# Optimization experiments

Hardware: AMD Instinct MI355X
Metric: run time of the kernel (lower is better)

The kernel has to match this reference:

```python
import jax, jax.numpy as jnp
import numpy as np

H = 512; VT = 10000; VN = 1000; ET = 256; EN = 256
A = 50; B = 8; L = 128; SOS = 0


def setup_inputs():
    key = jax.random.key(0)
    ks = jax.random.split(key, 12)
    g = lambda k, s: jax.random.normal(k, s, jnp.float32) * 0.02
    inp = {}
    inp["n_tensor"] = jax.random.randint(ks[0], (B, L), 0, VN)
    inp["t_tensor"] = jax.random.randint(ks[1], (B, L), 0, VT)
    inp["p_tensor"] = jax.random.randint(ks[2], (B, L), 0, L)
    # embedding tables; padding rows (padding_idx) zeroed as nn.Embedding init does
    inp["embN"] = g(ks[3], (VN, EN)).at[VN - 1].set(0.0)
    inp["embT"] = g(ks[4], (VT + A + 3, ET)).at[VT - 1].set(0.0)
    inp["W_hid"] = g(ks[5], (H, H)); inp["b_hid"] = jnp.zeros((H,), jnp.float32)
    inp["W_mem"] = g(ks[6], (H, H)); inp["b_mem"] = jnp.zeros((H,), jnp.float32)
    inp["v_w"] = g(ks[7], (H,)); inp["v_b"] = jnp.zeros((), jnp.float32)
    inp["W_ih"] = g(ks[8], (4 * H, EN + ET)); inp["W_hh"] = g(ks[9], (4 * H, H))
    inp["b_ih"] = jnp.zeros((4 * H,), jnp.float32); inp["b_hh"] = jnp.zeros((4 * H,), jnp.float32)
    inp["W_g"] = g(ks[10], (3 * H, VT + 3)); inp["b_g"] = jnp.zeros((VT + 3,), jnp.float32)
    inp["W_s"] = g(ks[11], (2 * H,)); inp["b_s"] = jnp.zeros((), jnp.float32)
    return inp


def _forward(embN, embT, W_hid, b_hid, W_mem, b_mem, v_w, v_b,
             W_ih, W_hh, b_ih, b_hh, W_g, b_g, W_s, b_s,
             n_tensor, t_tensor, p_tensor):
    full_mask = (n_tensor == VN - 1)                      # [B, L] eof mask
    sos = jnp.full((B, 1), SOS, n_tensor.dtype)
    n_in = jnp.concatenate([sos, n_tensor[:, :-1]], 1)    # teacher-forced inputs
    t_in = jnp.concatenate([sos, t_tensor[:, :-1]], 1)
    par = jnp.concatenate([jnp.zeros((B, 1), p_tensor.dtype), p_tensor[:, :-1]], 1)
    hs0 = jnp.zeros((B, L, H), jnp.float32)               # growing memory buffer
    h0 = jnp.zeros((B, H), jnp.float32)
    c0 = jnp.zeros((B, H), jnp.float32)
    barange = jnp.arange(B)
    arangeA = jnp.arange(A)

    def step(carry, xs):
        hs, h, c = carry
        t, n_t, t_t, p_t, tgt = xs
        # embedding gathers + single-layer LSTM cell (torch gate order i,f,g,o)
        x = jnp.concatenate([embN[n_t], embT[t_t]], 1)    # [B, EN+ET]
        gates = x @ W_ih.T + h @ W_hh.T + (b_ih + b_hh)
        i, f, gg, o = jnp.split(gates, 4, axis=1)
        c = jax.nn.sigmoid(f) * c + jax.nn.sigmoid(i) * jnp.tanh(gg)
        h = jax.nn.sigmoid(o) * jnp.tanh(c)
        # sliding-window memory hs[:, max(t-A,0):t], fixed-size slice + validity mask
        s = jnp.maximum(t - A, 0)
        mem = jax.lax.dynamic_slice(hs, (0, s, 0), (B, A, H))   # [B, A, H]
        fm = jax.lax.dynamic_slice(full_mask, (0, s), (B, A))   # [B, A]
        valid = (s + arangeA) < t                               # [A] positions already written
        mask = fm | ~valid[None, :]
        # additive attention: v^T tanh(W_hid h + W_mem mem)
        sc = jnp.tanh((h @ W_hid.T + b_hid)[:, None, :] + mem @ W_mem.T + b_mem)
        sc = sc @ v_w + v_b                                     # [B, A]
        sc = jnp.where(mask, -1e20, sc)
        attn = jax.nn.softmax(sc, axis=1)
        context = jnp.einsum('ba,bah->bh', attn, mem)
        h_parent = hs[barange, p_t]                             # per-batch gather on memory
        wt = jax.nn.log_softmax(jnp.concatenate([context, h, h_parent], 1) @ W_g + b_g, axis=1)
        log_attn = jax.nn.log_softmax(sc, axis=1)
        st = jax.nn.log_sigmoid(jnp.concatenate([context, h], 1) @ W_s + b_s)[:, None]  # [B,1]
        out = jnp.concatenate(
            [st + wt, jnp.log(jnp.clip(-jnp.expm1(st), 1e-18, 1e18)) + log_attn], 1)    # [B, VT+3+A]
        hs = hs.at[:, t].set(h)                                 # scatter new hidden into buffer
        loss_t = -jnp.take_along_axis(out, tgt[:, None], axis=1)[:, 0]  # NLLLoss(reduction='none')
        pred = jnp.argmax(out, axis=1)
        return (hs, h, c), (loss_t, pred)

    ts = jnp.arange(L)
    _, (losses, preds) = jax.lax.scan(
        step, (hs0, h0, c0), (ts, n_in.T, t_in.T, par.T, t_tensor.T))
    return losses.sum(), preds.T


def reference(n_tensor, t_tensor, p_tensor, embN, embT, W_hid, b_hid, W_mem, b_mem,
              v_w, v_b, W_ih, W_hh, b_ih, b_hh, W_g, b_g, W_s, b_s):
    return _forward(embN, embT, W_hid, b_hid, W_mem, b_mem, v_w, v_b,
                    W_ih, W_hh, b_ih, b_hh, W_g, b_g, W_s, b_s,
                    n_tensor, t_tensor, p_tensor)
```

## Files before the change

kernel.cpp:

```cpp
#include <hip/hip_runtime.h>
#include <hip/hip_bf16.h>
#include <math.h>

#define H_ 512
#define VN_ 1000
#define NG_ 10003
#define NGP_ 10240
#define NCHUNK 40
#define A_ 50
#define B_ 8
#define L_ 128
#define R_ 1024

typedef __hip_bfloat16 bf16;
typedef __attribute__((ext_vector_type(8))) short bf16x8;
typedef __attribute__((ext_vector_type(4))) float f32x4;

typedef union { unsigned long long u[2]; bf16x8 v; } frag_u;

__device__ __forceinline__ float fsig(float x) { return 1.0f / (1.0f + __expf(-x)); }
__device__ __forceinline__ float ftanh(float x) { return 1.0f - 2.0f / (1.0f + __expf(2.0f * x)); }

__device__ __forceinline__ short b16(float v) {
    __hip_bfloat16 h = __float2bfloat16(v);
    return *(short*)&h;
}

__device__ __forceinline__ unsigned long long ald(const unsigned long long* p) {
    return __hip_atomic_load(p, __ATOMIC_RELAXED, __HIP_MEMORY_SCOPE_AGENT);
}
__device__ __forceinline__ void ast32(unsigned int* p, unsigned int v) {
    __hip_atomic_store(p, v, __ATOMIC_RELAXED, __HIP_MEMORY_SCOPE_AGENT);
}

__global__ void k_init(int* flags, float* bkq,
                       const float* __restrict__ bmem, const float* __restrict__ bhid,
                       float* out)
{
    int i = blockIdx.x * 256 + threadIdx.x;
    if (i < 32)
        __hip_atomic_store(&flags[i], 0, __ATOMIC_RELAXED, __HIP_MEMORY_SCOPE_AGENT);
    if (i < 512) bkq[i] = bmem[i];
    else if (i < 1024) bkq[i] = bhid[i - 512];
    if (i == 0) out[0] = 0.f;
}

__global__ void k_w2b(const float* __restrict__ src, bf16* __restrict__ dst, int n)
{
    for (int i = blockIdx.x * blockDim.x + threadIdx.x; i < n; i += gridDim.x * blockDim.x)
        dst[i] = __float2bfloat16(src[i]);
}

__global__ void k_embed(const int* __restrict__ nt, const int* __restrict__ tt,
                        const float* __restrict__ embN, const float* __restrict__ embT,
                        bf16* __restrict__ X)
{
    int i = blockIdx.x * blockDim.x + threadIdx.x;
    int r = i >> 9, k = i & 511;
    int t = r >> 3, b = r & 7;
    float v;
    if (k < 256) {
        int id = (t == 0) ? 0 : nt[b * L_ + t - 1];
        v = embN[id * 256 + k];
    } else {
        int id = (t == 0) ? 0 : tt[b * L_ + t - 1];
        v = embT[id * 256 + (k - 256)];
    }
    X[i] = __float2bfloat16(v);
}

#define LSTM_BLOCKS 16
#define XTRA 240

#define DECLW(i) bf16x8 Wa##i, Wb##i;
#define LOADW(i) { \
    float4 a0 = *(const float4*)(wr0 + (i)*32); \
    float4 a1 = *(const float4*)(wr0 + (i)*32 + 4); \
    float4 c0 = *(const float4*)(wr1 + (i)*32); \
    float4 c1 = *(const float4*)(wr1 + (i)*32 + 4); \
    Wa##i[0]=b16(a0.x); Wa##i[1]=b16(a0.y); Wa##i[2]=b16(a0.z); Wa##i[3]=b16(a0.w); \
    Wa##i[4]=b16(a1.x); Wa##i[5]=b16(a1.y); Wa##i[6]=b16(a1.z); Wa##i[7]=b16(a1.w); \
    Wb##i[0]=b16(c0.x); Wb##i[1]=b16(c0.y); Wb##i[2]=b16(c0.z); Wb##i[3]=b16(c0.w); \
    Wb##i[4]=b16(c1.x); Wb##i[5]=b16(c1.y); Wb##i[6]=b16(c1.z); Wb##i[7]=b16(c1.w); }
#define LDF(i) frag_u fu##i; fu##i.u[0] = ald(src + (i)*128); fu##i.u[1] = ald(src + (i)*128 + 1);
#define MM(i) \
    acc0 = __builtin_amdgcn_mfma_f32_16x16x32_bf16(Wa##i, fu##i.v, acc0, 0, 0, 0); \
    acc1 = __builtin_amdgcn_mfma_f32_16x16x32_bf16(Wb##i, fu##i.v, acc1, 0, 0, 0);

__launch_bounds__(256, 1)
__global__ void k_lstm(const float* __restrict__ Whh, const float* __restrict__ xg,
                       bf16* __restrict__ hsb,
                       unsigned long long* __restrict__ bfr, int* __restrict__ flags,
                       const float* __restrict__ Wg, bf16* __restrict__ WT,
                       const float* __restrict__ Wmem, const float* __restrict__ Whid,
                       bf16* __restrict__ wkq)
{
    __shared__ float gl[4][32][9];
    __shared__ short S[64][65];
    const int tid  = threadIdx.x;
    const int x    = blockIdx.x;

    if (x >= LSTM_BLOCKS) {
        for (int i = (x - LSTM_BLOCKS) * 256 + tid; i < 2 * 512 * 512; i += XTRA * 256) {
            float v = (i < 512 * 512) ? Wmem[i] : Whid[i - 512 * 512];
            wkq[i] = __float2bfloat16(v);
        }
        const int c = tid & 63;
        const int r0 = (tid >> 6) * 16;
        const int n_l = tid >> 2;
        const int kq = (tid & 3) * 16;
        for (int tile = x - LSTM_BLOCKS; tile < 160 * 24; tile += XTRA) {
            int n0 = (tile % 160) * 64, k0 = (tile / 160) * 64;
            __syncthreads();
            #pragma unroll
            for (int i = 0; i < 16; ++i) {
                int k = r0 + i;
                int n = n0 + c;
                float v = (n < NG_) ? Wg[(size_t)(k0 + k) * NG_ + n] : 0.f;
                S[c][k] = b16(v);
            }
            __syncthreads();
            bf16* dst = WT + (size_t)(n0 + n_l) * 1536 + k0 + kq;
            #pragma unroll
            for (int j = 0; j < 2; ++j) {
                bf16x8 v;
                #pragma unroll
                for (int e = 0; e < 8; ++e) v[e] = S[n_l][kq + j * 8 + e];
                *(bf16x8*)(dst + j * 8) = v;
            }
        }
        return;
    }

    const int lane = tid & 63;
    const int w    = tid >> 6;
    const int m_l  = lane & 15;
    const int kg   = lane >> 4;
    const int n    = lane & 15;
    unsigned int* bfr32 = (unsigned int*)bfr;

    const float* wr0 = Whh + (size_t)(w * 512 + x * 32 + m_l) * 512 + kg * 8;
    const float* wr1 = wr0 + (size_t)16 * 512;
    DECLW(0)  DECLW(1)  DECLW(2)  DECLW(3)  DECLW(4)  DECLW(5)  DECLW(6)  DECLW(7)
    DECLW(8)  DECLW(9)  DECLW(10) DECLW(11) DECLW(12) DECLW(13) DECLW(14) DECLW(15)
    LOADW(0)  LOADW(1)  LOADW(2)  LOADW(3)  LOADW(4)  LOADW(5)  LOADW(6)  LOADW(7)
    LOADW(8)  LOADW(9)  LOADW(10) LOADW(11) LOADW(12) LOADW(13) LOADW(14) LOADW(15)
    asm volatile("" : "+v"(Wa0), "+v"(Wb0), "+v"(Wa1), "+v"(Wb1), "+v"(Wa2), "+v"(Wb2),
                      "+v"(Wa3), "+v"(Wb3), "+v"(Wa4), "+v"(Wb4), "+v"(Wa5), "+v"(Wb5),
                      "+v"(Wa6), "+v"(Wb6), "+v"(Wa7), "+v"(Wb7));
    asm volatile("" : "+v"(Wa8), "+v"(Wb8), "+v"(Wa9), "+v"(Wb9), "+v"(Wa10), "+v"(Wb10),
                      "+v"(Wa11), "+v"(Wb11), "+v"(Wa12), "+v"(Wb12), "+v"(Wa13), "+v"(Wb13),
                      "+v"(Wa14), "+v"(Wb14), "+v"(Wa15), "+v"(Wb15));

    const int u_l = tid >> 3;
    const int b   = tid & 7;
    float creg = 0.f;
    int fearly = 0;

    for (int t = 0; t < L_; ++t) {
        const float* xr = xg + ((size_t)t * B_ + b) * 2048 + x * 32 + u_l;
        float xi = xr[0], xf = xr[512], xgg = xr[1024], xo = xr[1536];

        f32x4 acc0 = {0.f, 0.f, 0.f, 0.f};
        f32x4 acc1 = {0.f, 0.f, 0.f, 0.f};
        if (t > 0) {
            if (!__all(fearly >= t)) {
                for (;;) {
                    int v = (lane < LSTM_BLOCKS)
                        ? __hip_atomic_load(&flags[lane], __ATOMIC_RELAXED, __HIP_MEMORY_SCOPE_AGENT)
                        : t;
                    if (__all(v >= t)) break;
                    __builtin_amdgcn_s_sleep(1);
                }
            }
            const unsigned long long* src =
                bfr + (size_t)((t + 1) & 1) * 2048 + lane * 2;
            LDF(0)  LDF(1)  LDF(2)  LDF(3)  LDF(4)  LDF(5)  LDF(6)  LDF(7)
            LDF(8)  LDF(9)  LDF(10) LDF(11) LDF(12) LDF(13) LDF(14) LDF(15)
            __builtin_amdgcn_sched_barrier(0);
            MM(0)  MM(1)  MM(2)  MM(3)  MM(4)  MM(5)  MM(6)  MM(7)
            MM(8)  MM(9)  MM(10) MM(11) MM(12) MM(13) MM(14) MM(15)
        }
        if (n < 8) {
            #pragma unroll
            for (int i = 0; i < 4; ++i) {
                gl[w][kg * 4 + i][n]      = acc0[i];
                gl[w][16 + kg * 4 + i][n] = acc1[i];
            }
        }
        __syncthreads();
        float gi = gl[0][u_l][b] + xi;
        float gf = gl[1][u_l][b] + xf;
        float gg = gl[2][u_l][b] + xgg;
        float go = gl[3][u_l][b] + xo;
        float iv = fsig(gi), fv = fsig(gf), gv = ftanh(gg), ov = fsig(go);
        creg = fv * creg + iv * gv;
        float h = ov * ftanh(creg);
        float h2 = __shfl_xor(h, 8);
        unsigned pay = 0;
        if ((u_l & 1) == 0) {
            pay = (unsigned)(unsigned short)b16(h)
                | ((unsigned)(unsigned short)b16(h2) << 16);
            int q = u_l >> 3, p = (u_l & 7) >> 1;
            ast32(bfr32 + (size_t)(t & 1) * 4096 + x * 256 + (b + 16 * q) * 4 + p, pay);
        }
        fearly = (lane < LSTM_BLOCKS && lane != x)
            ? __hip_atomic_load(&flags[lane], __ATOMIC_RELAXED, __HIP_MEMORY_SCOPE_AGENT)
            : 0x7FFFFFFF;
        asm volatile("s_waitcnt vmcnt(0)" ::: "memory");
        __syncthreads();
        if (tid == 0)
            __hip_atomic_store(&flags[x], t + 1, __ATOMIC_RELAXED, __HIP_MEMORY_SCOPE_AGENT);
        if ((u_l & 1) == 0)
            *(unsigned int*)(hsb + (size_t)(t * B_ + b) * 512 + x * 32 + u_l) = pay;
    }
}

__launch_bounds__(256)
__global__ void k_attn(const bf16* __restrict__ hsb, const float* __restrict__ kmq,
                       const float* __restrict__ vw,
                       const float* __restrict__ vb, const int* __restrict__ nt,
                       const int* __restrict__ pt, const float* __restrict__ Wsv,
                       const float* __restrict__ bs, bf16* __restrict__ gcat,
                       float* __restrict__ logattn, float* __restrict__ stbuf)
{
    const int r = blockIdx.x;
    const int t = r >> 3, b = r & 7;
    const int tid = threadIdx.x;
    const int lane = tid & 63, wave = tid >> 6;
    int s = t - A_; if (s < 0) s = 0;
    __shared__ float qv[512];
    __shared__ float vwl[512];
    __shared__ float sc[A_];
    __shared__ float attn[A_];
    __shared__ float red[4];
    for (int i = tid; i < 512; i += 256) {
        qv[i] = kmq[(size_t)r * 1024 + 512 + i];
        vwl[i] = vw[i];
    }
    __syncthreads();
    for (int a = wave; a < A_; a += 4) {
        int pos = s + a;
        float v = -1e20f;
        bool masked = (pos >= t) || (nt[b * L_ + pos] == VN_ - 1);
        if (!masked) {
            const float* kr = kmq + (size_t)(pos * B_ + b) * 1024;
            float p = 0.f;
            for (int k = lane; k < 512; k += 64)
                p += vwl[k] * ftanh(qv[k] + kr[k]);
            for (int off = 32; off; off >>= 1) p += __shfl_down(p, off);
            v = p + vb[0];
        }
        if (lane == 0) sc[a] = v;
    }
    __syncthreads();
    if (tid < 64) {
        float v = (tid < A_) ? sc[tid] : -INFINITY;
        float m = v;
        for (int off = 32; off; off >>= 1) m = fmaxf(m, __shfl_xor(m, off));
        float e = (tid < A_) ? expf(v - m) : 0.f;
        float d = e;
        for (int off = 32; off; off >>= 1) d += __shfl_xor(d, off);
        if (tid < A_) {
            attn[tid] = e / d;
            logattn[(size_t)r * A_ + tid] = (v - m) - logf(d);
        }
    }
    __syncthreads();
    const int k0 = tid * 2;
    float c0 = 0.f, c1 = 0.f;
    for (int a = 0; a < A_; ++a) {
        int pos = s + a;
        if (pos >= t) break;
        float w = attn[a];
        unsigned u = *(const unsigned*)((const unsigned short*)hsb + (size_t)(pos * B_ + b) * 512 + k0);
        c0 += w * __uint_as_float(u << 16);
        c1 += w * __uint_as_float(u & 0xffff0000u);
    }
    unsigned ucur = *(const unsigned*)((const unsigned short*)hsb + (size_t)(t * B_ + b) * 512 + k0);
    int par = (t == 0) ? 0 : pt[b * L_ + t - 1];
    unsigned upar = 0;
    if (par < t)
        upar = *(const unsigned*)((const unsigned short*)hsb + (size_t)(par * B_ + b) * 512 + k0);
    float hx = __uint_as_float(ucur << 16), hy = __uint_as_float(ucur & 0xffff0000u);
    bf16* g = gcat + (size_t)r * 1536;
    g[k0]     = __float2bfloat16(c0);
    g[k0 + 1] = __float2bfloat16(c1);
    *(unsigned*)(g + 512 + k0)  = ucur;
    *(unsigned*)(g + 1024 + k0) = upar;
    float part = c0 * Wsv[k0] + c1 * Wsv[k0 + 1]
               + hx * Wsv[512 + k0] + hy * Wsv[512 + k0 + 1];
    for (int off = 32; off; off >>= 1) part += __shfl_down(part, off);
    if (lane == 0) red[wave] = part;
    __syncthreads();
    if (tid == 0) {
        float z = red[0] + red[1] + red[2] + red[3] + bs[0];
        stbuf[r] = -log1pf(expf(-z));
    }
}

__launch_bounds__(256, 2)
__global__ void k_gemm128b(const bf16* __restrict__ Ag, const bf16* __restrict__ Bg,
                           const float* __restrict__ b1, const float* __restrict__ b2,
                           float* __restrict__ C, int N, int K)
{
    __shared__ short As[128 * 32];
    __shared__ short Bs[128 * 32];
    const int tid = threadIdx.x;
    const int lane = tid & 63, wave = tid >> 6;
    const int wr = wave >> 1, wc = wave & 1;
    const int m0 = blockIdx.y * 128, n0 = blockIdx.x * 128;
    f32x4 acc[4][4] = {};
    for (int k0 = 0; k0 < K; k0 += 32) {
        __syncthreads();
        #pragma unroll
        for (int h = 0; h < 2; ++h) {
            int o = tid + h * 256;
            int row = o >> 2;
            int kc = (o & 3) ^ (row & 3);
            const bf16* ga = Ag + (size_t)(m0 + row) * K + k0 + kc * 8;
            const bf16* gb = Bg + (size_t)(n0 + row) * K + k0 + kc * 8;
            unsigned ldso = h * 4096 + wave * 1024;
            __builtin_amdgcn_global_load_lds(
                (const __attribute__((address_space(1))) void*)ga,
                (__attribute__((address_space(3))) void*)((char*)As + ldso), 16, 0, 0);
            __builtin_amdgcn_global_load_lds(
                (const __attribute__((address_space(1))) void*)gb,
                (__attribute__((address_space(3))) void*)((char*)Bs + ldso), 16, 0, 0);
        }
        asm volatile("s_waitcnt vmcnt(0)" ::: "memory");
        __syncthreads();
        bf16x8 af[4], bf[4];
        #pragma unroll
        for (int mi = 0; mi < 4; ++mi) {
            int ra = wr * 64 + mi * 16 + (lane & 15);
            af[mi] = *(const bf16x8*)&As[ra * 32 + (((lane >> 4) ^ (ra & 3)) * 8)];
        }
        #pragma unroll
        for (int ni = 0; ni < 4; ++ni) {
            int rb = wc * 64 + ni * 16 + (lane & 15);
            bf[ni] = *(const bf16x8*)&Bs[rb * 32 + (((lane >> 4) ^ (rb & 3)) * 8)];
        }
        #pragma unroll
        for (int mi = 0; mi < 4; ++mi)
            #pragma unroll
            for (int ni = 0; ni < 4; ++ni)
                acc[mi][ni] = __builtin_amdgcn_mfma_f32_16x16x32_bf16(af[mi], bf[ni], acc[mi][ni], 0, 0, 0);
    }
    const int col = lane & 15, rq = (lane >> 4) * 4;
    #pragma unroll
    for (int mi = 0; mi < 4; ++mi)
        #pragma unroll
        for (int ni = 0; ni < 4; ++ni) {
            int nn = n0 + wc * 64 + ni * 16 + col;
            float bias = (b1 ? b1[nn] : 0.f) + (b2 ? b2[nn] : 0.f);
            #pragma unroll
            for (int i = 0; i < 4; ++i)
                C[(size_t)(m0 + wr * 64 + mi * 16 + rq + i) * N + nn] = acc[mi][ni][i] + bias;
        }
}

__launch_bounds__(256, 2)
__global__ void k_gemm128p(const bf16* __restrict__ Ag, const bf16* __restrict__ Bg,
                           const float* __restrict__ bg, const int* __restrict__ tt,
                           float* __restrict__ pst)
{
    __shared__ short As[128 * 32];
    __shared__ short Bs[128 * 32];
    __shared__ float bgl[256];
    __shared__ float mrg[128][6];
    const int tid = threadIdx.x;
    const int lane = tid & 63, wave = tid >> 6;
    const int wr = wave >> 1, wc = wave & 1;
    const int col16 = lane & 15, rq = (lane >> 4) * 4;
    const int chunk = blockIdx.x;
    const int m0 = blockIdx.y * 128;
    const int K = 1536;

    bgl[tid] = (chunk * 256 + tid < NG_) ? bg[chunk * 256 + tid] : -INFINITY;

    float M[4][4], S[4][4], AV[4][4], TGT[4][4]; int AI[4][4]; int tgt[4][4];
    #pragma unroll
    for (int mi = 0; mi < 4; ++mi)
        #pragma unroll
        for (int i = 0; i < 4; ++i) {
            M[mi][i] = -INFINITY; S[mi][i] = 0.f; AV[mi][i] = -INFINITY;
            TGT[mi][i] = -INFINITY; AI[mi][i] = 0x7FFFFFFF;
            int row = m0 + wr * 64 + mi * 16 + rq + i;
            tgt[mi][i] = tt[(row & 7) * L_ + (row >> 3)];
        }

    for (int nt = 0; nt < 2; ++nt) {
        const int n0 = chunk * 256 + nt * 128;
        f32x4 acc[4][4] = {};
        for (int k0 = 0; k0 < K; k0 += 32) {
            __syncthreads();
            #pragma unroll
            for (int h = 0; h < 2; ++h) {
                int o = tid + h * 256;
                int row = o >> 2;
                int kc = (o & 3) ^ (row & 3);
                const bf16* ga = Ag + (size_t)(m0 + row) * K + k0 + kc * 8;
                const bf16* gb = Bg + (size_t)(n0 + row) * K + k0 + kc * 8;
                unsigned ldso = h * 4096 + wave * 1024;
                __builtin_amdgcn_global_load_lds(
                    (const __attribute__((address_space(1))) void*)ga,
                    (__attribute__((address_space(3))) void*)((char*)As + ldso), 16, 0, 0);
                __builtin_amdgcn_global_load_lds(
                    (const __attribute__((address_space(1))) void*)gb,
                    (__attribute__((address_space(3))) void*)((char*)Bs + ldso), 16, 0, 0);
            }
            asm volatile("s_waitcnt vmcnt(0)" ::: "memory");
            __syncthreads();
            bf16x8 af[4], bf[4];
            #pragma unroll
            for (int mi = 0; mi < 4; ++mi) {
                int ra = wr * 64 + mi * 16 + col16;
                af[mi] = *(const bf16x8*)&As[ra * 32 + (((lane >> 4) ^ (ra & 3)) * 8)];
            }
            #pragma unroll
            for (int ni = 0; ni < 4; ++ni) {
                int rb = wc * 64 + ni * 16 + col16;
                bf[ni] = *(const bf16x8*)&Bs[rb * 32 + (((lane >> 4) ^ (rb & 3)) * 8)];
            }
            #pragma unroll
            for (int mi = 0; mi < 4; ++mi)
                #pragma unroll
                for (int ni = 0; ni < 4; ++ni)
                    acc[mi][ni] = __builtin_amdgcn_mfma_f32_16x16x32_bf16(af[mi], bf[ni], acc[mi][ni], 0, 0, 0);
        }
        #pragma unroll
        for (int mi = 0; mi < 4; ++mi)
            #pragma unroll
            for (int i = 0; i < 4; ++i) {
                float v[4]; int nn[4];
                #pragma unroll
                for (int ni = 0; ni < 4; ++ni) {
                    int cl = nt * 128 + wc * 64 + ni * 16 + col16;
                    v[ni] = acc[mi][ni][i] + bgl[cl];
                    nn[ni] = chunk * 256 + cl;
                }
                float lv = v[0]; int li = nn[0];
                #pragma unroll
                for (int ni = 1; ni < 4; ++ni)
                    if (v[ni] > lv) { lv = v[ni]; li = nn[ni]; }
                #pragma unroll
                for (int off = 1; off < 16; off <<= 1) {
                    float ov = __shfl_xor(lv, off); int oi = __shfl_xor(li, off);
                    if (ov > lv || (ov == lv && oi < li)) { lv = ov; li = oi; }
                }
                float nM = fmaxf(M[mi][i], lv);
                float add = 0.f;
                if (nM != -INFINITY) {
                    #pragma unroll
                    for (int ni = 0; ni < 4; ++ni) add += expf(v[ni] - nM);
                    #pragma unroll
                    for (int off = 1; off < 16; off <<= 1) add += __shfl_xor(add, off);
                }
                S[mi][i] = ((S[mi][i] > 0.f) ? S[mi][i] * expf(M[mi][i] - nM) : 0.f) + add;
                M[mi][i] = nM;
                if (lv > AV[mi][i] || (lv == AV[mi][i] && li < AI[mi][i])) {
                    AV[mi][i] = lv; AI[mi][i] = li;
                }
                float tv = -INFINITY;
                #pragma unroll
                for (int ni = 0; ni < 4; ++ni)
                    if (nn[ni] == tgt[mi][i]) tv = v[ni];
                #pragma unroll
                for (int off = 1; off < 16; off <<= 1)
                    tv = fmaxf(tv, __shfl_xor(tv, off));
                TGT[mi][i] = fmaxf(TGT[mi][i], tv);
            }
    }
    __syncthreads();
    if (wc == 1 && col16 == 0) {
        #pragma unroll
        for (int mi = 0; mi < 4; ++mi)
            #pragma unroll
            for (int i = 0; i < 4; ++i) {
                int rl = wr * 64 + mi * 16 + rq + i;
                mrg[rl][0] = M[mi][i]; mrg[rl][1] = S[mi][i];
                mrg[rl][2] = AV[mi][i]; mrg[rl][3] = __int_as_float(AI[mi][i]);
                mrg[rl][4] = TGT[mi][i];
            }
    }
    __syncthreads();
    if (wc == 0 && col16 == 0) {
        #pragma unroll
        for (int mi = 0; mi < 4; ++mi)
            #pragma unroll
            for (int i = 0; i < 4; ++i) {
                int rl = wr * 64 + mi * 16 + rq + i;
                float oM = mrg[rl][0], oS = mrg[rl][1], oAV = mrg[rl][2];
                int oAI = __float_as_int(mrg[rl][3]);
                float oT = mrg[rl][4];
                float nM = fmaxf(M[mi][i], oM);
                float s1 = (S[mi][i] > 0.f) ? S[mi][i] * expf(M[mi][i] - nM) : 0.f;
                float s2 = (oS > 0.f) ? oS * expf(oM - nM) : 0.f;
                float av = AV[mi][i]; int ai = AI[mi][i];
                if (oAV > av || (oAV == av && oAI < ai)) { av = oAV; ai = oAI; }
                float* p = pst + ((size_t)chunk * R_ + (m0 + rl)) * 8;
                p[0] = nM; p[1] = s1 + s2; p[2] = av;
                p[3] = __int_as_float(ai); p[4] = fmaxf(TGT[mi][i], oT);
            }
    }
}

__launch_bounds__(64)
__global__ void k_loss2(const float* __restrict__ pst, const float* __restrict__ logattn,
                        const float* __restrict__ stbuf, float* __restrict__ out)
{
    const int r = blockIdx.x;
    const int lane = threadIdx.x;
    float M = -INFINITY, S = 0.f, AV = -INFINITY, TGT = -INFINITY;
    int AI = 0x7FFFFFFF;
    if (lane < NCHUNK) {
        const float* p = pst + ((size_t)lane * R_ + r) * 8;
        M = p[0]; S = p[1]; AV = p[2]; AI = __float_as_int(p[3]); TGT = p[4];
    }
    for (int off = 32; off; off >>= 1) {
        float oM = __shfl_xor(M, off), oS = __shfl_xor(S, off);
        float oAV = __shfl_xor(AV, off), oT = __shfl_xor(TGT, off);
        int oAI = __shfl_xor(AI, off);
        float nM = fmaxf(M, oM);
        float s1 = (S > 0.f) ? S * expf(M - nM) : 0.f;
        float s2 = (oS > 0.f) ? oS * expf(oM - nM) : 0.f;
        M = nM; S = s1 + s2;
        if (oAV > AV || (oAV == AV && oAI < AI)) { AV = oAV; AI = oAI; }
        TGT = fmaxf(TGT, oT);
    }
    if (lane == 0) {
        float lse = M + logf(S);
        float st = stbuf[r];
        const float* la = logattn + (size_t)r * A_;
        float lamax = la[0]; int aidx = 0;
        for (int a = 1; a < A_; ++a) if (la[a] > lamax) { lamax = la[a]; aidx = a; }
        float e1 = -expm1f(st);
        e1 = fminf(fmaxf(e1, 1e-18f), 1e18f);
        float lm = logf(e1);
        float p1 = st + M - lse;
        float p2 = lm + lamax;
        int pred = (p1 >= p2) ? AI : (NG_ + aidx);
        float loss = -(st + TGT - lse);
        atomicAdd(&out[0], loss);
        int t = r >> 3, b = r & 7;
        out[1 + b * L_ + t] = (float)pred;
    }
}

extern "C" void kernel_launch(void* const* d_in, const int* in_sizes, int n_in,
                              void* d_out, int out_size, void* d_ws, size_t ws_size,
                              hipStream_t stream)
{
    (void)in_sizes; (void)n_in; (void)out_size; (void)ws_size;
    const int*   nt    = (const int*)d_in[0];
    const int*   tt    = (const int*)d_in[1];
    const int*   pt    = (const int*)d_in[2];
    const float* embN  = (const float*)d_in[3];
    const float* embT  = (const float*)d_in[4];
    const float* W_hid = (const float*)d_in[5];
    const float* b_hid = (const float*)d_in[6];
    const float* W_mem = (const float*)d_in[7];
    const float* b_mem = (const float*)d_in[8];
    const float* v_w   = (const float*)d_in[9];
    const float* v_b   = (const float*)d_in[10];
    const float* W_ih  = (const float*)d_in[11];
    const float* W_hh  = (const float*)d_in[12];
    const float* b_ih  = (const float*)d_in[13];
    const float* b_hh  = (const float*)d_in[14];
    const float* W_g   = (const float*)d_in[15];
    const float* b_g   = (const float*)d_in[16];
    const float* W_s   = (const float*)d_in[17];
    const float* b_s   = (const float*)d_in[18];
    float* out = (float*)d_out;

    char* ws = (char*)d_ws;
    size_t o = 0;
    bf16*  WGT  = (bf16*)(ws + o);  o += (size_t)NGP_ * 1536 * 2;
    float* XG   = (float*)(ws + o); o += (size_t)R_ * 2048 * 4;
    bf16*  HSB  = (bf16*)(ws + o);  o += (size_t)R_ * H_ * 2;
    float* KMQ  = (float*)(ws + o); o += (size_t)R_ * 1024 * 4;
    bf16*  WKQ  = (bf16*)(ws + o);  o += (size_t)1024 * 512 * 2;
    float* BKQ  = (float*)(ws + o); o += (size_t)1024 * 4;
    bf16*  XB   = (bf16*)(ws + o);  o += (size_t)R_ * H_ * 2;
    bf16*  WIHB = (bf16*)(ws + o);  o += (size_t)2048 * 512 * 2;
    bf16*  GC   = (bf16*)(ws + o);  o += (size_t)R_ * 1536 * 2;
    float* LA   = (float*)(ws + o); o += (size_t)R_ * A_ * 4;
    float* ST   = (float*)(ws + o); o += (size_t)R_ * 4;
    float* PST  = (float*)(ws + o); o += (size_t)NCHUNK * R_ * 8 * 4;
    unsigned long long* BFR = (unsigned long long*)(ws + o); o += (size_t)4096 * 8;
    int*   FLG  = (int*)(ws + o);   o += 256;

    k_init<<<4, 256, 0, stream>>>(FLG, BKQ, b_mem, b_hid, out);
    k_w2b<<<1024, 256, 0, stream>>>(W_ih, WIHB, 2048 * 512);
    k_embed<<<R_ * H_ / 256, 256, 0, stream>>>(nt, tt, embN, embT, XB);
    k_gemm128b<<<dim3(2048 / 128, R_ / 128), 256, 0, stream>>>(XB, WIHB, b_ih, b_hh, XG, 2048, 512);
    k_lstm<<<LSTM_BLOCKS + XTRA, 256, 0, stream>>>(W_hh, XG, HSB, BFR, FLG,
                                                   W_g, WGT, W_mem, W_hid, WKQ);
    k_gemm128b<<<dim3(1024 / 128, R_ / 128), 256, 0, stream>>>(HSB, WKQ, BKQ, nullptr, KMQ, 1024, 512);
    k_attn<<<R_, 256, 0, stream>>>(HSB, KMQ, v_w, v_b, nt, pt, W_s, b_s, GC, LA, ST);
    k_gemm128p<<<dim3(NCHUNK, R_ / 128), 256, 0, stream>>>(GC, WGT, b_g, tt, PST);
    k_loss2<<<R_, 64, 0, stream>>>(PST, LA, ST, out);
}
```

Baseline: 603.8 us.

## Fuse prep kernels into one launch and split vocab GEMM into more chunks

```diff
diff --git a/kernel.cpp b/kernel.cpp
--- a/kernel.cpp
+++ b/kernel.cpp
@@ -6,7 +6,7 @@
 #define VN_ 1000
 #define NG_ 10003
 #define NGP_ 10240
-#define NCHUNK 40
+#define NCHUNK 80
 #define A_ 50
 #define B_ 8
 #define L_ 128
@@ -29,44 +29,45 @@
 __device__ __forceinline__ unsigned long long ald(const unsigned long long* p) {
     return __hip_atomic_load(p, __ATOMIC_RELAXED, __HIP_MEMORY_SCOPE_AGENT);
 }
+__device__ __forceinline__ int aldi(const int* p) {
+    return __hip_atomic_load(p, __ATOMIC_RELAXED, __HIP_MEMORY_SCOPE_AGENT);
+}
 __device__ __forceinline__ void ast32(unsigned int* p, unsigned int v) {
     __hip_atomic_store(p, v, __ATOMIC_RELAXED, __HIP_MEMORY_SCOPE_AGENT);
 }
-
-__global__ void k_init(int* flags, float* bkq,
+__device__ __forceinline__ void asti(int* p, int v) {
+    __hip_atomic_store(p, v, __ATOMIC_RELAXED, __HIP_MEMORY_SCOPE_AGENT);
+}
+
+__global__ void k_prep(int* flags, float* bkq,
                        const float* __restrict__ bmem, const float* __restrict__ bhid,
-                       float* out)
+                       float* out,
+                       const float* __restrict__ Wih, bf16* __restrict__ wihb,
+                       const int* __restrict__ nt, const int* __restrict__ tt,
+                       const float* __restrict__ embN, const float* __restrict__ embT,
+                       bf16* __restrict__ X)
 {
-    int i = blockIdx.x * 256 + threadIdx.x;
+    const int i = blockIdx.x * 256 + threadIdx.x;
+    const int total = gridDim.x * 256;
     if (i < 32)
         __hip_atomic_store(&flags[i], 0, __ATOMIC_RELAXED, __HIP_MEMORY_SCOPE_AGENT);
-    if (i < 512) bkq[i] = bmem[i];
-    else if (i < 1024) bkq[i] = bhid[i - 512];
+    if (i < 1024) bkq[i] = (i < 512) ? bmem[i] : bhid[i - 512];
     if (i == 0) out[0] = 0.f;
-}
-
-__global__ void k_w2b(const float* __restrict__ src, bf16* __restrict__ dst, int n)
-{
-    for (int i = blockIdx.x * blockDim.x + threadIdx.x; i < n; i += gridDim.x * blockDim.x)
-        dst[i] = __float2bfloat16(src[i]);
-}
-
-__global__ void k_embed(const int* __restrict__ nt, const int* __restrict__ tt,
-                        const float* __restrict__ embN, const float* __restrict__ embT,
-                        bf16* __restrict__ X)
-{
-    int i = blockIdx.x * blockDim.x + threadIdx.x;
-    int r = i >> 9, k = i & 511;
-    int t = r >> 3, b = r & 7;
-    float v;
-    if (k < 256) {
-        int id = (t == 0) ? 0 : nt[b * L_ + t - 1];
-        v = embN[id * 256 + k];
-    } else {
-        int id = (t == 0) ? 0 : tt[b * L_ + t - 1];
-        v = embT[id * 256 + (k - 256)];
-    }
-    X[i] = __float2bfloat16(v);
+    for (int j = i; j < 2048 * 512; j += total)
+        wihb[j] = __float2bfloat16(Wih[j]);
+    {
+        int r = i >> 9, k = i & 511;
+        int t = r >> 3, b = r & 7;
+        float v;
+        if (k < 256) {
+            int id = (t == 0) ? 0 : nt[b * L_ + t - 1];
+            v = embN[id * 256 + k];
+        } else {
+            int id = (t == 0) ? 0 : tt[b * L_ + t - 1];
+            v = embT[id * 256 + (k - 256)];
+        }
+        X[i] = __float2bfloat16(v);
+    }
 }
 
 #define LSTM_BLOCKS 16
@@ -166,9 +167,7 @@
         if (t > 0) {
             if (!__all(fearly >= t)) {
                 for (;;) {
-                    int v = (lane < LSTM_BLOCKS)
-                        ? __hip_atomic_load(&flags[lane], __ATOMIC_RELAXED, __HIP_MEMORY_SCOPE_AGENT)
-                        : t;
+                    int v = (lane < LSTM_BLOCKS) ? aldi(&flags[lane]) : t;
                     if (__all(v >= t)) break;
                     __builtin_amdgcn_s_sleep(1);
                 }
@@ -204,13 +203,11 @@
             int q = u_l >> 3, p = (u_l & 7) >> 1;
             ast32(bfr32 + (size_t)(t & 1) * 4096 + x * 256 + (b + 16 * q) * 4 + p, pay);
         }
-        fearly = (lane < LSTM_BLOCKS && lane != x)
-            ? __hip_atomic_load(&flags[lane], __ATOMIC_RELAXED, __HIP_MEMORY_SCOPE_AGENT)
-            : 0x7FFFFFFF;
+        fearly = (lane < LSTM_BLOCKS && lane != x) ? aldi(&flags[lane]) : 0x7FFFFFFF;
         asm volatile("s_waitcnt vmcnt(0)" ::: "memory");
         __syncthreads();
         if (tid == 0)
-            __hip_atomic_store(&flags[x], t + 1, __ATOMIC_RELAXED, __HIP_MEMORY_SCOPE_AGENT);
+            asti(&flags[x], t + 1);
         if ((u_l & 1) == 0)
             *(unsigned int*)(hsb + (size_t)(t * B_ + b) * 512 + x * 32 + u_l) = pay;
     }
@@ -367,7 +364,7 @@
 {
     __shared__ short As[128 * 32];
     __shared__ short Bs[128 * 32];
-    __shared__ float bgl[256];
+    __shared__ float bgl[128];
     __shared__ float mrg[128][6];
     const int tid = threadIdx.x;
     const int lane = tid & 63, wave = tid >> 6;
@@ -375,9 +372,10 @@
     const int col16 = lane & 15, rq = (lane >> 4) * 4;
     const int chunk = blockIdx.x;
     const int m0 = blockIdx.y * 128;
+    const int n0 = chunk * 128;
     const int K = 1536;
 
-    bgl[tid] = (chunk * 256 + tid < NG_) ? bg[chunk * 256 + tid] : -INFINITY;
+    if (tid < 128) bgl[tid] = (n0 + tid < NG_) ? bg[n0 + tid] : -INFINITY;
 
     float M[4][4], S[4][4], AV[4][4], TGT[4][4]; int AI[4][4]; int tgt[4][4];
     #pragma unroll
@@ -390,88 +388,82 @@
             tgt[mi][i] = tt[(row & 7) * L_ + (row >> 3)];
         }
 
-    for (int nt = 0; nt < 2; ++nt) {
-        const int n0 = chunk * 256 + nt * 128;
-        f32x4 acc[4][4] = {};
-        for (int k0 = 0; k0 < K; k0 += 32) {
-            __syncthreads();
-            #pragma unroll
-            for (int h = 0; h < 2; ++h) {
-                int o = tid + h * 256;
-                int row = o >> 2;
-                int kc = (o & 3) ^ (row & 3);
-                const bf16* ga = Ag + (size_t)(m0 + row) * K + k0 + kc * 8;
-                const bf16* gb = Bg + (size_t)(n0 + row) * K + k0 + kc * 8;
-                unsigned ldso = h * 4096 + wave * 1024;
-                __builtin_amdgcn_global_load_lds(
-                    (const __attribute__((address_space(1))) void*)ga,
-                    (__attribute__((address_space(3))) void*)((char*)As + ldso), 16, 0, 0);
-                __builtin_amdgcn_global_load_lds(
-                    (const __attribute__((address_space(1))) void*)gb,
-                    (__attribute__((address_space(3))) void*)((char*)Bs + ldso), 16, 0, 0);
-            }
-            asm volatile("s_waitcnt vmcnt(0)" ::: "memory");
-            __syncthreads();
-            bf16x8 af[4], bf[4];
-            #pragma unroll
-            for (int mi = 0; mi < 4; ++mi) {
-                int ra = wr * 64 + mi * 16 + col16;
-                af[mi] = *(const bf16x8*)&As[ra * 32 + (((lane >> 4) ^ (ra & 3)) * 8)];
-            }
+    f32x4 acc[4][4] = {};
+    for (int k0 = 0; k0 < K; k0 += 32) {
+        __syncthreads();
+        #pragma unroll
+        for (int h = 0; h < 2; ++h) {
+            int o = tid + h * 256;
+            int row = o >> 2;
+            int kc = (o & 3) ^ (row & 3);
+            const bf16* ga = Ag + (size_t)(m0 + row) * K + k0 + kc * 8;
+            const bf16* gb = Bg + (size_t)(n0 + row) * K + k0 + kc * 8;
+            unsigned ldso = h * 4096 + wave * 1024;
+            __builtin_amdgcn_global_load_lds(
+                (const __attribute__((address_space(1))) void*)ga,
+                (__attribute__((address_space(3))) void*)((char*)As + ldso), 16, 0, 0);
+            __builtin_amdgcn_global_load_lds(
+                (const __attribute__((address_space(1))) void*)gb,
+                (__attribute__((address_space(3))) void*)((char*)Bs + ldso), 16, 0, 0);
+        }
+        asm volatile("s_waitcnt vmcnt(0)" ::: "memory");
+        __syncthreads();
+        bf16x8 af[4], bf[4];
+        #pragma unroll
+        for (int mi = 0; mi < 4; ++mi) {
+            int ra = wr * 64 + mi * 16 + col16;
+            af[mi] = *(const bf16x8*)&As[ra * 32 + (((lane >> 4) ^ (ra & 3)) * 8)];
+        }
+        #pragma unroll
+        for (int ni = 0; ni < 4; ++ni) {
+            int rb = wc * 64 + ni * 16 + col16;
+            bf[ni] = *(const bf16x8*)&Bs[rb * 32 + (((lane >> 4) ^ (rb & 3)) * 8)];
+        }
+        #pragma unroll
+        for (int mi = 0; mi < 4; ++mi)
+            #pragma unroll
+            for (int ni = 0; ni < 4; ++ni)
+                acc[mi][ni] = __builtin_amdgcn_mfma_f32_16x16x32_bf16(af[mi], bf[ni], acc[mi][ni], 0, 0, 0);
+    }
+    #pragma unroll
+    for (int mi = 0; mi < 4; ++mi)
+        #pragma unroll
+        for (int i = 0; i < 4; ++i) {
+            float v[4]; int nn[4];
             #pragma unroll
             for (int ni = 0; ni < 4; ++ni) {
-                int rb = wc * 64 + ni * 16 + col16;
-                bf[ni] = *(const bf16x8*)&Bs[rb * 32 + (((lane >> 4) ^ (rb & 3)) * 8)];
-            }
-            #pragma unroll
-            for (int mi = 0; mi < 4; ++mi)
+                int cl = wc * 64 + ni * 16 + col16;
+                v[ni] = acc[mi][ni][i] + bgl[cl];
+                nn[ni] = n0 + cl;
+            }
+            float lv = v[0]; int li = nn[0];
+            #pragma unroll
+            for (int ni = 1; ni < 4; ++ni)
+                if (v[ni] > lv) { lv = v[ni]; li = nn[ni]; }
+            #pragma unroll
+            for (int off = 1; off < 16; off <<= 1) {
+                float ov = __shfl_xor(lv, off); int oi = __shfl_xor(li, off);
+                if (ov > lv || (ov == lv && oi < li)) { lv = ov; li = oi; }
+            }
+            float nM = lv;
+            float add = 0.f;
+            if (nM != -INFINITY) {
                 #pragma unroll
-                for (int ni = 0; ni < 4; ++ni)
-                    acc[mi][ni] = __builtin_amdgcn_mfma_f32_16x16x32_bf16(af[mi], bf[ni], acc[mi][ni], 0, 0, 0);
-        }
-        #pragma unroll
-        for (int mi = 0; mi < 4; ++mi)
-            #pragma unroll
-            for (int i = 0; i < 4; ++i) {
-                float v[4]; int nn[4];
+                for (int ni = 0; ni < 4; ++ni) add += expf(v[ni] - nM);
                 #pragma unroll
-                for (int ni = 0; ni < 4; ++ni) {
-                    int cl = nt * 128 + wc * 64 + ni * 16 + col16;
-                    v[ni] = acc[mi][ni][i] + bgl[cl];
-                    nn[ni] = chunk * 256 + cl;
-                }
-                float lv = v[0]; int li = nn[0];
-                #pragma unroll
-                for (int ni = 1; ni < 4; ++ni)
-                    if (v[ni] > lv) { lv = v[ni]; li = nn[ni]; }
-                #pragma unroll
-                for (int off = 1; off < 16; off <<= 1) {
-                    float ov = __shfl_xor(lv, off); int oi = __shfl_xor(li, off);
-                    if (ov > lv || (ov == lv && oi < li)) { lv = ov; li = oi; }
-                }
-                float nM = fmaxf(M[mi][i], lv);
-                float add = 0.f;
-                if (nM != -INFINITY) {
-                    #pragma unroll
-                    for (int ni = 0; ni < 4; ++ni) add += expf(v[ni] - nM);
-                    #pragma unroll
-                    for (int off = 1; off < 16; off <<= 1) add += __shfl_xor(add, off);
-                }
-                S[mi][i] = ((S[mi][i] > 0.f) ? S[mi][i] * expf(M[mi][i] - nM) : 0.f) + add;
-                M[mi][i] = nM;
-                if (lv > AV[mi][i] || (lv == AV[mi][i] && li < AI[mi][i])) {
-                    AV[mi][i] = lv; AI[mi][i] = li;
-                }
-                float tv = -INFINITY;
-                #pragma unroll
-                for (int ni = 0; ni < 4; ++ni)
-                    if (nn[ni] == tgt[mi][i]) tv = v[ni];
-                #pragma unroll
-                for (int off = 1; off < 16; off <<= 1)
-                    tv = fmaxf(tv, __shfl_xor(tv, off));
-                TGT[mi][i] = fmaxf(TGT[mi][i], tv);
-            }
-    }
+                for (int off = 1; off < 16; off <<= 1) add += __shfl_xor(add, off);
+            }
+            M[mi][i] = nM; S[mi][i] = add;
+            AV[mi][i] = lv; AI[mi][i] = li;
+            float tv = -INFINITY;
+            #pragma unroll
+            for (int ni = 0; ni < 4; ++ni)
+                if (nn[ni] == tgt[mi][i]) tv = v[ni];
+            #pragma unroll
+            for (int off = 1; off < 16; off <<= 1)
+                tv = fmaxf(tv, __shfl_xor(tv, off));
+            TGT[mi][i] = tv;
+        }
     __syncthreads();
     if (wc == 1 && col16 == 0) {
         #pragma unroll
@@ -514,9 +506,17 @@
     const int lane = threadIdx.x;
     float M = -INFINITY, S = 0.f, AV = -INFINITY, TGT = -INFINITY;
     int AI = 0x7FFFFFFF;
-    if (lane < NCHUNK) {
-        const float* p = pst + ((size_t)lane * R_ + r) * 8;
-        M = p[0]; S = p[1]; AV = p[2]; AI = __float_as_int(p[3]); TGT = p[4];
+    for (int c = lane; c < NCHUNK; c += 64) {
+        const float* p = pst + ((size_t)c * R_ + r) * 8;
+        float oM = p[0], oS = p[1], oAV = p[2];
+        int oAI = __float_as_int(p[3]);
+        float oT = p[4];
+        float nM = fmaxf(M, oM);
+        float s1 = (S > 0.f) ? S * expf(M - nM) : 0.f;
+        float s2 = (oS > 0.f) ? oS * expf(oM - nM) : 0.f;
+        M = nM; S = s1 + s2;
+        if (oAV > AV || (oAV == AV && oAI < AI)) { AV = oAV; AI = oAI; }
+        TGT = fmaxf(TGT, oT);
     }
     for (int off = 32; off; off >>= 1) {
         float oM = __shfl_xor(M, off), oS = __shfl_xor(S, off);
@@ -591,9 +591,8 @@
     unsigned long long* BFR = (unsigned long long*)(ws + o); o += (size_t)4096 * 8;
     int*   FLG  = (int*)(ws + o);   o += 256;
 
-    k_init<<<4, 256, 0, stream>>>(FLG, BKQ, b_mem, b_hid, out);
-    k_w2b<<<1024, 256, 0, stream>>>(W_ih, WIHB, 2048 * 512);
-    k_embed<<<R_ * H_ / 256, 256, 0, stream>>>(nt, tt, embN, embT, XB);
+    k_prep<<<2048, 256, 0, stream>>>(FLG, BKQ, b_mem, b_hid, out,
+                                     W_ih, WIHB, nt, tt, embN, embT, XB);
     k_gemm128b<<<dim3(2048 / 128, R_ / 128), 256, 0, stream>>>(XB, WIHB, b_ih, b_hh, XG, 2048, 512);
     k_lstm<<<LSTM_BLOCKS + XTRA, 256, 0, stream>>>(W_hh, XG, HSB, BFR, FLG,
                                                    W_g, WGT, W_mem, W_hid, WKQ);
```

Result: faster. 563.4 us, median of 2 (-6.7%).
